# Optimization experiments

Hardware: AMD Instinct MI355X
Metric: run time of the kernel (lower is better)

Reference implementation:

```python
import jax, jax.numpy as jnp
import numpy as np

B, T, C = 2, 8192, 1024
H, BS, LW = 16, 64, 128          # num_heads, block_size, local_window_size
D = C // H                        # head_dim = 64
W = BS + LW                       # max window length per block = 192
NB = T // BS                      # number of blocks


def setup_inputs() -> dict:
    key = jax.random.key(0)
    ks = jax.random.split(key, 11)
    s = 1.0 / np.sqrt(C)          # small init so softmax is not saturated
    return {
        'query': jax.random.normal(ks[0], (B, T, C), jnp.float32),
        'key':   jax.random.normal(ks[1], (B, T, C), jnp.float32),
        'value': jax.random.normal(ks[2], (B, T, C), jnp.float32),
        'Wq': jax.random.normal(ks[3], (C, C), jnp.float32) * s,
        'bq': jax.random.normal(ks[4], (C,), jnp.float32) * s,
        'Wk': jax.random.normal(ks[5], (C, C), jnp.float32) * s,
        'bk': jax.random.normal(ks[6], (C,), jnp.float32) * s,
        'Wv': jax.random.normal(ks[7], (C, C), jnp.float32) * s,
        'bv': jax.random.normal(ks[8], (C,), jnp.float32) * s,
        'Wo': jax.random.normal(ks[9], (C, C), jnp.float32) * s,
        'bo': jax.random.normal(ks[10], (C,), jnp.float32) * s,
    }


def reference(query, key, value, Wq, bq, Wk, bk, Wv, bv, Wo, bo):
    # projections -> (B, H, T, D)
    def proj(x, Wt, bt):
        return (x @ Wt.T + bt).reshape(B, T, H, D).transpose(0, 2, 1, 3)

    scale = jnp.asarray(D, query.dtype) ** -0.5
    q = proj(query, Wq, bq) * scale
    k = proj(key, Wk, bk)
    v = proj(value, Wv, bv)

    # per-block window indices: block i attends to [i - LW//2, i + BS + LW//2)
    starts = jnp.arange(NB) * BS                              # (NB,)
    idx = starts[:, None] + jnp.arange(-LW // 2, BS + LW // 2)  # (NB, W)
    valid = (idx >= 0) & (idx < T)                            # (NB, W)
    cidx = jnp.clip(idx, 0, T - 1)

    q_blk = q.reshape(B, H, NB, BS, D)
    k_win = k[:, :, cidx, :]                                  # (B, H, NB, W, D)
    v_win = v[:, :, cidx, :]

    scores = jnp.einsum('bhnqd,bhnkd->bhnqk', q_blk, k_win).astype(jnp.float32)
    scores = jnp.where(valid[None, None, :, None, :], scores, -jnp.inf)
    probs = jax.nn.softmax(scores, axis=-1).astype(q.dtype)

    out = jnp.einsum('bhnqk,bhnkd->bhnqd', probs, v_win)      # (B, H, NB, BS, D)
    out = out.reshape(B, H, T, D).transpose(0, 2, 1, 3).reshape(B, T, C)
    return out @ Wo.T + bo
```

## Files before the change

kernel.cpp:

```cpp
#include <hip/hip_runtime.h>
#include <hip/hip_bf16.h>
#include <type_traits>

#define BATCH 2
#define SEQ   8192
#define CH    1024
#define NH    16
#define BLK   64
#define WIN   192
#define NBL   128
#define DH    64
#define MR    (BATCH*SEQ)

typedef __bf16 bf16x8 __attribute__((ext_vector_type(8)));
typedef float  f32x4  __attribute__((ext_vector_type(4)));

__device__ __forceinline__ f32x4 zero4() {
    f32x4 z; z[0]=0.f; z[1]=0.f; z[2]=0.f; z[3]=0.f; return z;
}

union Pack8 { __hip_bfloat16 h[8]; uint4 u; };
union Pack4 { __hip_bfloat16 h[4]; uint2 u; };

typedef const __attribute__((address_space(1))) unsigned int* gas_ptr;
typedef       __attribute__((address_space(3))) unsigned int* las_ptr;

__device__ __forceinline__ void gload_lds16(const __hip_bfloat16* g, __hip_bfloat16* l) {
    __builtin_amdgcn_global_load_lds((gas_ptr)(const void*)g, (las_ptr)(void*)l, 16, 0, 0);
}

__device__ __forceinline__ int xcd_swz(int bid, int nwg) {
    return (bid & 7) * (nwg >> 3) + (bid >> 3);
}

__global__ __launch_bounds__(256) void pack_all(
    const float* __restrict__ q,  const float* __restrict__ k,
    const float* __restrict__ v,
    const float* __restrict__ wq, const float* __restrict__ wk,
    const float* __restrict__ wv, const float* __restrict__ wo,
    __hip_bfloat16* __restrict__ xq, __hip_bfloat16* __restrict__ xk,
    __hip_bfloat16* __restrict__ xv,
    __hip_bfloat16* __restrict__ wqb, __hip_bfloat16* __restrict__ wkb,
    __hip_bfloat16* __restrict__ wvb, __hip_bfloat16* __restrict__ wob)
{
    const int NA8B = (MR * CH / 8) / 256;
    const int NW8B = (CH * CH / 8) / 256;
    int bid = blockIdx.x;
    const float* src;
    __hip_bfloat16* dst;
    int rel;
    if (bid < 3 * NA8B) {
        int t = bid / NA8B; rel = bid - t * NA8B;
        src = (t == 0) ? q : (t == 1) ? k : v;
        dst = (t == 0) ? xq : (t == 1) ? xk : xv;
    } else {
        int b2 = bid - 3 * NA8B;
        int t = b2 / NW8B; rel = b2 - t * NW8B;
        src = (t == 0) ? wq : (t == 1) ? wk : (t == 2) ? wv : wo;
        dst = (t == 0) ? wqb : (t == 1) ? wkb : (t == 2) ? wvb : wob;
    }
    const int base = rel * 512;
    const float4* s = reinterpret_cast<const float4*>(src);
    uint2* d = reinterpret_cast<uint2*>(dst);
    float4 a = s[base + threadIdx.x];
    float4 b = s[base + 256 + threadIdx.x];
    Pack4 pa, pb;
    pa.h[0] = __float2bfloat16(a.x); pa.h[1] = __float2bfloat16(a.y);
    pa.h[2] = __float2bfloat16(a.z); pa.h[3] = __float2bfloat16(a.w);
    pb.h[0] = __float2bfloat16(b.x); pb.h[1] = __float2bfloat16(b.y);
    pb.h[2] = __float2bfloat16(b.z); pb.h[3] = __float2bfloat16(b.w);
    d[base + threadIdx.x]       = pa.u;
    d[base + 256 + threadIdx.x] = pb.u;
}


__device__ __forceinline__ void stage_half(
    const __hip_bfloat16* __restrict__ g, int goff,
    __hip_bfloat16* sm, int loff, int tid)
{
    gload_lds16(g + goff,            sm + loff + tid * 8);
    gload_lds16(g + goff + 128 * CH, sm + loff + (tid + 512) * 8);
}

#define SB0 __builtin_amdgcn_sched_barrier(0)
#define LGKM0 do { asm volatile("s_waitcnt lgkmcnt(0)" ::: "memory"); \
                   __builtin_amdgcn_sched_barrier(0); } while (0)
#define VMCNT(n) do { asm volatile("s_waitcnt vmcnt(" #n ")" ::: "memory"); \
                      __builtin_amdgcn_sched_barrier(0); } while (0)

template<int MH, bool RB>
__device__ __forceinline__ void phase_reads(
    const __hip_bfloat16* Ak, const __hip_bfloat16* Bk,
    int aoff, int boff, bf16x8 (&af)[4], bf16x8 (&bfk)[4])
{
    if constexpr (RB) {
        #pragma unroll
        for (int j = 0; j < 4; ++j)
            bfk[j] = *reinterpret_cast<const bf16x8*>(Bk + boff + j * 512);
    }
    #pragma unroll
    for (int i = 0; i < 4; ++i)
        af[i] = *reinterpret_cast<const bf16x8*>(Ak + aoff + (MH * 4 + i) * 512);
}

template<int MH>
__device__ __forceinline__ void phase_mfma16(
    const bf16x8 (&af)[4], const bf16x8 (&bfk)[4], f32x4 (&acc)[8][4])
{
    __builtin_amdgcn_s_setprio(1);
    #pragma unroll
    for (int i = 0; i < 4; ++i)
        #pragma unroll
        for (int j = 0; j < 4; ++j)
            acc[MH * 4 + i][j] = __builtin_amdgcn_mfma_f32_16x16x32_bf16(
                af[i], bfk[j], acc[MH * 4 + i][j], 0, 0, 0);
    __builtin_amdgcn_s_setprio(0);
}

template<typename OT>
__device__ __forceinline__ void gemm_body256(
    const __hip_bfloat16* __restrict__ A, const __hip_bfloat16* __restrict__ Wb,
    const float* __restrict__ bias, OT* __restrict__ out, float alpha,
    int m0, int n0, __hip_bfloat16* sm)
{
    const int tid  = threadIdx.x;
    const int wid  = tid >> 6;
    const int lane = tid & 63;
    const int quad = lane >> 4;
    const int l16  = lane & 15;
    const int wr   = wid >> 2, wc = wid & 3;

    const int r0 = tid >> 2;
    const int s0 = (tid & 3) ^ ((tid >> 3) & 3);
    const int offA0 = (m0 + r0) * CH + s0 * 8;
    const int offB0 = (n0 + r0) * CH + s0 * 8;

    const int cq   = quad ^ ((l16 >> 1) & 3);
    const int aoff = ((wr * 128 + l16) * 4 + cq) * 8;
    const int boff = ((wc * 64  + l16) * 4 + cq) * 8;

    f32x4 acc[8][4];
    #pragma unroll
    for (int i = 0; i < 8; ++i)
        #pragma unroll
        for (int j = 0; j < 4; ++j) acc[i][j] = zero4();

    stage_half(A,  offA0,      sm, 0,             tid);
    stage_half(Wb, offB0,      sm, 32768,         tid);
    stage_half(A,  offA0 + 32, sm, 8192,          tid);
    stage_half(Wb, offB0 + 32, sm, 32768 + 8192,  tid);
    VMCNT(4);
    __builtin_amdgcn_s_barrier();
    SB0;

    bf16x8 af[4], bfk[4];

    #pragma unroll 1
    for (int t = 0; t < 15; ++t) {
        const int cur = t & 1, nb = cur ^ 1;
        const int kn  = (t + 1) * 64;
        const __hip_bfloat16* As_ = sm + cur * 16384;
        const __hip_bfloat16* Bs_ = sm + 32768 + cur * 16384;

        phase_reads<0, true>(As_, Bs_, aoff, boff, af, bfk);
        stage_half(A, offA0 + kn, sm, nb * 16384, tid);
        SB0;
        __builtin_amdgcn_s_barrier();
        LGKM0;
        phase_mfma16<0>(af, bfk, acc);
        __builtin_amdgcn_s_barrier();

        phase_reads<1, false>(As_, Bs_, aoff, boff, af, bfk);
        stage_half(Wb, offB0 + kn, sm, 32768 + nb * 16384, tid);
        SB0;
        __builtin_amdgcn_s_barrier();
        LGKM0;
        phase_mfma16<1>(af, bfk, acc);
        VMCNT(4);
        __builtin_amdgcn_s_barrier();

        phase_reads<0, true>(As_ + 8192, Bs_ + 8192, aoff, boff, af, bfk);
        stage_half(A, offA0 + kn + 32, sm, nb * 16384 + 8192, tid);
        SB0;
        __builtin_amdgcn_s_barrier();
        LGKM0;
        phase_mfma16<0>(af, bfk, acc);
        __builtin_amdgcn_s_barrier();

        phase_reads<1, false>(As_ + 8192, Bs_ + 8192, aoff, boff, af, bfk);
        stage_half(Wb, offB0 + kn + 32, sm, 32768 + nb * 16384 + 8192, tid);
        SB0;
        __builtin_amdgcn_s_barrier();
        LGKM0;
        phase_mfma16<1>(af, bfk, acc);
        VMCNT(4);
        __builtin_amdgcn_s_barrier();
    }

    {
        const __hip_bfloat16* As_ = sm + 16384;
        const __hip_bfloat16* Bs_ = sm + 32768 + 16384;

        phase_reads<0, true>(As_, Bs_, aoff, boff, af, bfk);
        SB0;
        __builtin_amdgcn_s_barrier();
        LGKM0;
        phase_mfma16<0>(af, bfk, acc);
        __builtin_amdgcn_s_barrier();

        phase_reads<1, false>(As_, Bs_, aoff, boff, af, bfk);
        SB0;
        __builtin_amdgcn_s_barrier();
        LGKM0;
        phase_mfma16<1>(af, bfk, acc);
        VMCNT(0);
        __builtin_amdgcn_s_barrier();

        phase_reads<0, true>(As_ + 8192, Bs_ + 8192, aoff, boff, af, bfk);
        SB0;
        __builtin_amdgcn_s_barrier();
        LGKM0;
        phase_mfma16<0>(af, bfk, acc);
        __builtin_amdgcn_s_barrier();

        phase_reads<1, false>(As_ + 8192, Bs_ + 8192, aoff, boff, af, bfk);
        SB0;
        __builtin_amdgcn_s_barrier();
        LGKM0;
        phase_mfma16<1>(af, bfk, acc);
    }

    #pragma unroll
    for (int j = 0; j < 4; ++j) {
        const int col = n0 + wc * 64 + j * 16 + l16;
        const float bv = bias[col];
        #pragma unroll
        for (int i = 0; i < 8; ++i) {
            #pragma unroll
            for (int r = 0; r < 4; ++r) {
                const int row = m0 + wr * 128 + i * 16 + quad * 4 + r;
                float v = alpha * (acc[i][j][r] + bv);
                if constexpr (std::is_same<OT, float>::value)
                    out[(size_t)row * CH + col] = v;
                else
                    out[(size_t)row * CH + col] = __float2bfloat16(v);
            }
        }
    }
}

__device__ __forceinline__ void gemm_tile256(int& m0, int& n0) {
    int bid = blockIdx.y * 4 + blockIdx.x;
    int swz = (bid & 7) * 32 + (bid >> 3);
    m0 = (swz >> 2) * 256;
    n0 = (swz & 3) * 256;
}

__global__ __launch_bounds__(512, 2) void gemm_qk256(
    const __hip_bfloat16* __restrict__ A0, const __hip_bfloat16* __restrict__ W0,
    const float* __restrict__ b0, __hip_bfloat16* __restrict__ o0, float alpha0,
    const __hip_bfloat16* __restrict__ A1, const __hip_bfloat16* __restrict__ W1,
    const float* __restrict__ b1, __hip_bfloat16* __restrict__ o1)
{
    __shared__ alignas(16) __hip_bfloat16 sm[65536];
    int m0, n0; gemm_tile256(m0, n0);
    if (blockIdx.z == 0)
        gemm_body256<__hip_bfloat16>(A0, W0, b0, o0, alpha0, m0, n0, sm);
    else
        gemm_body256<__hip_bfloat16>(A1, W1, b1, o1, 1.0f, m0, n0, sm);
}

template<typename OT>
__global__ __launch_bounds__(512, 2) void gemm_one256(
    const __hip_bfloat16* __restrict__ A, const __hip_bfloat16* __restrict__ Wb,
    const float* __restrict__ bias, OT* __restrict__ out)
{
    __shared__ alignas(16) __hip_bfloat16 sm[65536];
    int m0, n0; gemm_tile256(m0, n0);
    gemm_body256<OT>(A, Wb, bias, out, 1.0f, m0, n0, sm);
}

__global__ __launch_bounds__(256, 3) void attn_kernel(
    const __hip_bfloat16* __restrict__ qg,
    const __hip_bfloat16* __restrict__ kg,
    const __hip_bfloat16* __restrict__ vg,
    __hip_bfloat16* __restrict__ ctx)
{
    __shared__ alignas(16) char smem[53248];
    auto ks = reinterpret_cast<__hip_bfloat16(*)[72]>(smem);
    auto vt = reinterpret_cast<__hip_bfloat16(*)[200]>(smem + 27648);
    auto ps = reinterpret_cast<__hip_bfloat16(*)[200]>(smem);

    const int blk = xcd_swz(blockIdx.x, BATCH * NH * NBL);
    const int n = blk & (NBL - 1);
    const int h = (blk >> 7) & (NH - 1);
    const int b = blk >> 11;
    const int t0  = n * BLK;
    const int kst = t0 - 64;
    const int tid = threadIdx.x;
    const size_t baseBH = (size_t)b * SEQ * CH + (size_t)h * DH;

    const int wid = tid >> 6, lane = tid & 63, quad = lane >> 4, l16 = lane & 15;

    const __hip_bfloat16* qrow = qg + baseBH + (size_t)(t0 + wid * 16 + l16) * CH + quad * 8;
    bf16x8 aq0 = *reinterpret_cast<const bf16x8*>(qrow);
    bf16x8 aq1 = *reinterpret_cast<const bf16x8*>(qrow + 32);

    uint4 vreg[6];
    int vj[6], vseg[6];
    #pragma unroll
    for (int it = 0; it < 6; it++) {
        int c = tid + it * 256;
        vj[it] = c % WIN; vseg[it] = c / WIN;
        int tr = kst + vj[it]; tr = tr < 0 ? 0 : (tr >= SEQ ? SEQ - 1 : tr);
        vreg[it] = *reinterpret_cast<const uint4*>(vg + baseBH + (size_t)tr * CH + vseg[it] * 8);
    }

    #pragma unroll
    for (int it = 0; it < 6; it++) {
        int c = tid + it * 256;
        int row = c >> 3, seg = c & 7;
        int tr = kst + row; tr = tr < 0 ? 0 : (tr >= SEQ ? SEQ - 1 : tr);
        *reinterpret_cast<uint4*>(&ks[row][seg * 8]) =
            *reinterpret_cast<const uint4*>(kg + baseBH + (size_t)tr * CH + seg * 8);
    }
    __syncthreads();

    f32x4 sc[12];
    #pragma unroll
    for (int j = 0; j < 12; j++) sc[j] = zero4();
    #pragma unroll
    for (int j = 0; j < 12; j++) {
        bf16x8 bk0 = *reinterpret_cast<const bf16x8*>(&ks[j * 16 + l16][quad * 8]);
        sc[j] = __builtin_amdgcn_mfma_f32_16x16x32_bf16(aq0, bk0, sc[j], 0, 0, 0);
        bf16x8 bk1 = *reinterpret_cast<const bf16x8*>(&ks[j * 16 + l16][32 + quad * 8]);
        sc[j] = __builtin_amdgcn_mfma_f32_16x16x32_bf16(aq1, bk1, sc[j], 0, 0, 0);
    }
    __syncthreads();

    #pragma unroll
    for (int it = 0; it < 6; it++) {
        Pack8 p; p.u = vreg[it];
        #pragma unroll
        for (int e = 0; e < 8; e++) vt[vseg[it] * 8 + e][vj[it]] = p.h[e];
    }

    #pragma unroll
    for (int r = 0; r < 4; r++) {
        float s[12];
        float mx = -3.0e38f;
        #pragma unroll
        for (int j = 0; j < 12; j++) {
            int col = j * 16 + l16;
            int tr = kst + col;
            bool valid = (tr >= 0) && (tr < SEQ);
            s[j] = valid ? sc[j][r] : -3.0e38f;
            mx = fmaxf(mx, s[j]);
        }
        #pragma unroll
        for (int o = 1; o < 16; o <<= 1) mx = fmaxf(mx, __shfl_xor(mx, o, 64));
        float sum = 0.f;
        #pragma unroll
        for (int j = 0; j < 12; j++) {
            float e = __expf(s[j] - mx);
            s[j] = e;
            sum += e;
        }
        #pragma unroll
        for (int o = 1; o < 16; o <<= 1) sum += __shfl_xor(sum, o, 64);
        const float inv = 1.f / sum;
        const int row = wid * 16 + quad * 4 + r;
        #pragma unroll
        for (int j = 0; j < 12; j++)
            ps[row][j * 16 + l16] = __float2bfloat16(s[j] * inv);
    }
    __syncthreads();

    f32x4 oa[4];
    #pragma unroll
    for (int j = 0; j < 4; j++) oa[j] = zero4();
    #pragma unroll
    for (int kk = 0; kk < 6; kk++) {
        bf16x8 ap = *reinterpret_cast<const bf16x8*>(&ps[wid * 16 + l16][kk * 32 + quad * 8]);
        #pragma unroll
        for (int j = 0; j < 4; j++) {
            bf16x8 bv = *reinterpret_cast<const bf16x8*>(&vt[j * 16 + l16][kk * 32 + quad * 8]);
            oa[j] = __builtin_amdgcn_mfma_f32_16x16x32_bf16(ap, bv, oa[j], 0, 0, 0);
        }
    }
    #pragma unroll
    for (int j = 0; j < 4; j++) {
        const int d = j * 16 + l16;
        #pragma unroll
        for (int r = 0; r < 4; r++) {
            const int i = wid * 16 + quad * 4 + r;
            ctx[baseBH + (size_t)(t0 + i) * CH + d] = __float2bfloat16(oa[j][r]);
        }
    }
}

extern "C" void kernel_launch(void* const* d_in, const int* in_sizes, int n_in,
                              void* d_out, int out_size, void* d_ws, size_t ws_size,
                              hipStream_t stream)
{
    const float* query = (const float*)d_in[0];
    const float* key_i = (const float*)d_in[1];
    const float* value = (const float*)d_in[2];
    const float* Wq = (const float*)d_in[3];
    const float* bq = (const float*)d_in[4];
    const float* Wk = (const float*)d_in[5];
    const float* bk = (const float*)d_in[6];
    const float* Wv = (const float*)d_in[7];
    const float* bv = (const float*)d_in[8];
    const float* Wo = (const float*)d_in[9];
    const float* bo = (const float*)d_in[10];
    float* out = (float*)d_out;

    const size_t NELEM = (size_t)MR * CH;
    const size_t WELEM = (size_t)CH * CH;

    __hip_bfloat16* S0 = (__hip_bfloat16*)d_ws;
    __hip_bfloat16* S1 = S0 + NELEM;
    __hip_bfloat16* S2 = S1 + NELEM;
    __hip_bfloat16* S3 = S2 + NELEM;
    __hip_bfloat16* wqb = S3;
    __hip_bfloat16* wkb = S3 + WELEM;
    __hip_bfloat16* wvb = S3 + 2 * WELEM;
    __hip_bfloat16* wob = S3 + 3 * WELEM;

    __hip_bfloat16* xq = (__hip_bfloat16*)d_out;
    __hip_bfloat16* xk = xq + NELEM;
    __hip_bfloat16* vb = (__hip_bfloat16*)d_out;
    __hip_bfloat16* qb = S1;
    __hip_bfloat16* kb = S2;
    __hip_bfloat16* cb = S0;

    const int NA8B = (int)((NELEM / 8) / 256);
    const int NW8B = (int)((WELEM / 8) / 256);

    pack_all<<<3 * NA8B + 4 * NW8B, 256, 0, stream>>>(
        query, key_i, value, Wq, Wk, Wv, Wo,
        xq, xk, S0, wqb, wkb, wvb, wob);

    dim3 ggrid(CH / 256, MR / 256);
    dim3 qkgrid(CH / 256, MR / 256, 2);

    gemm_qk256<<<qkgrid, 512, 0, stream>>>(xq, wqb, bq, qb, 0.125f,
                                           xk, wkb, bk, kb);
    gemm_one256<__hip_bfloat16><<<ggrid, 512, 0, stream>>>(S0, wvb, bv, vb);

    attn_kernel<<<BATCH * NH * NBL, 256, 0, stream>>>(qb, kb, vb, cb);

    gemm_one256<float><<<ggrid, 512, 0, stream>>>(cb, wob, bo, out);
}
```

Before: 425.3 us.

## Fuse fp32-to-bf16 activation conversion into projection GEMM A-tile staging

Result: slower. 451.7 us (+6.2%).

```diff
diff --git a/kernel.cpp b/kernel.cpp
--- a/kernel.cpp
+++ b/kernel.cpp
@@ -20,7 +20,6 @@
 }
 
 union Pack8 { __hip_bfloat16 h[8]; uint4 u; };
-union Pack4 { __hip_bfloat16 h[4]; uint2 u; };
 
 typedef const __attribute__((address_space(1))) unsigned int* gas_ptr;
 typedef       __attribute__((address_space(3))) unsigned int* las_ptr;
@@ -33,38 +32,23 @@
     return (bid & 7) * (nwg >> 3) + (bid >> 3);
 }
 
-__global__ __launch_bounds__(256) void pack_all(
-    const float* __restrict__ q,  const float* __restrict__ k,
-    const float* __restrict__ v,
+__global__ __launch_bounds__(256) void pack_w(
     const float* __restrict__ wq, const float* __restrict__ wk,
     const float* __restrict__ wv, const float* __restrict__ wo,
-    __hip_bfloat16* __restrict__ xq, __hip_bfloat16* __restrict__ xk,
-    __hip_bfloat16* __restrict__ xv,
     __hip_bfloat16* __restrict__ wqb, __hip_bfloat16* __restrict__ wkb,
     __hip_bfloat16* __restrict__ wvb, __hip_bfloat16* __restrict__ wob)
 {
-    const int NA8B = (MR * CH / 8) / 256;
     const int NW8B = (CH * CH / 8) / 256;
     int bid = blockIdx.x;
-    const float* src;
-    __hip_bfloat16* dst;
-    int rel;
-    if (bid < 3 * NA8B) {
-        int t = bid / NA8B; rel = bid - t * NA8B;
-        src = (t == 0) ? q : (t == 1) ? k : v;
-        dst = (t == 0) ? xq : (t == 1) ? xk : xv;
-    } else {
-        int b2 = bid - 3 * NA8B;
-        int t = b2 / NW8B; rel = b2 - t * NW8B;
-        src = (t == 0) ? wq : (t == 1) ? wk : (t == 2) ? wv : wo;
-        dst = (t == 0) ? wqb : (t == 1) ? wkb : (t == 2) ? wvb : wob;
-    }
+    int t = bid >> 9, rel = bid & (NW8B - 1);
+    const float* src = (t == 0) ? wq : (t == 1) ? wk : (t == 2) ? wv : wo;
+    __hip_bfloat16* dst = (t == 0) ? wqb : (t == 1) ? wkb : (t == 2) ? wvb : wob;
     const int base = rel * 512;
     const float4* s = reinterpret_cast<const float4*>(src);
     uint2* d = reinterpret_cast<uint2*>(dst);
     float4 a = s[base + threadIdx.x];
     float4 b = s[base + 256 + threadIdx.x];
-    Pack4 pa, pb;
+    union { __hip_bfloat16 h[4]; uint2 u; } pa, pb;
     pa.h[0] = __float2bfloat16(a.x); pa.h[1] = __float2bfloat16(a.y);
     pa.h[2] = __float2bfloat16(a.z); pa.h[3] = __float2bfloat16(a.w);
     pb.h[0] = __float2bfloat16(b.x); pb.h[1] = __float2bfloat16(b.y);
@@ -82,6 +66,31 @@
     gload_lds16(g + goff + 128 * CH, sm + loff + (tid + 512) * 8);
 }
 
+__device__ __forceinline__ void stageA32_load(
+    const float* __restrict__ g, int goff, float4 (&fr)[4])
+{
+    const float4* p0 = reinterpret_cast<const float4*>(g + goff);
+    const float4* p1 = reinterpret_cast<const float4*>(g + goff + 128 * CH);
+    fr[0] = p0[0]; fr[1] = p0[1];
+    fr[2] = p1[0]; fr[3] = p1[1];
+}
+
+__device__ __forceinline__ void stageA32_write(
+    const float4 (&fr)[4], __hip_bfloat16* sm, int loff, int tid)
+{
+    Pack8 pa, pb;
+    pa.h[0] = __float2bfloat16(fr[0].x); pa.h[1] = __float2bfloat16(fr[0].y);
+    pa.h[2] = __float2bfloat16(fr[0].z); pa.h[3] = __float2bfloat16(fr[0].w);
+    pa.h[4] = __float2bfloat16(fr[1].x); pa.h[5] = __float2bfloat16(fr[1].y);
+    pa.h[6] = __float2bfloat16(fr[1].z); pa.h[7] = __float2bfloat16(fr[1].w);
+    pb.h[0] = __float2bfloat16(fr[2].x); pb.h[1] = __float2bfloat16(fr[2].y);
+    pb.h[2] = __float2bfloat16(fr[2].z); pb.h[3] = __float2bfloat16(fr[2].w);
+    pb.h[4] = __float2bfloat16(fr[3].x); pb.h[5] = __float2bfloat16(fr[3].y);
+    pb.h[6] = __float2bfloat16(fr[3].z); pb.h[7] = __float2bfloat16(fr[3].w);
+    *reinterpret_cast<uint4*>(sm + loff + tid * 8)         = pa.u;
+    *reinterpret_cast<uint4*>(sm + loff + (tid + 512) * 8) = pb.u;
+}
+
 #define SB0 __builtin_amdgcn_sched_barrier(0)
 #define LGKM0 do { asm volatile("s_waitcnt lgkmcnt(0)" ::: "memory"); \
                    __builtin_amdgcn_sched_barrier(0); } while (0)
@@ -117,12 +126,14 @@
     __builtin_amdgcn_s_setprio(0);
 }
 
-template<typename OT>
+template<typename OT, typename AT>
 __device__ __forceinline__ void gemm_body256(
-    const __hip_bfloat16* __restrict__ A, const __hip_bfloat16* __restrict__ Wb,
+    const AT* __restrict__ A, const __hip_bfloat16* __restrict__ Wb,
     const float* __restrict__ bias, OT* __restrict__ out, float alpha,
     int m0, int n0, __hip_bfloat16* sm)
 {
+    constexpr bool A32 = std::is_same<AT, float>::value;
+
     const int tid  = threadIdx.x;
     const int wid  = tid >> 6;
     const int lane = tid & 63;
@@ -145,11 +156,24 @@
         #pragma unroll
         for (int j = 0; j < 4; ++j) acc[i][j] = zero4();
 
-    stage_half(A,  offA0,      sm, 0,             tid);
-    stage_half(Wb, offB0,      sm, 32768,         tid);
-    stage_half(A,  offA0 + 32, sm, 8192,          tid);
-    stage_half(Wb, offB0 + 32, sm, 32768 + 8192,  tid);
-    VMCNT(4);
+    float4 frA[4], frB[4];
+
+    if constexpr (A32) {
+        stageA32_load(A, offA0,      frA);
+        stageA32_load(A, offA0 + 32, frB);
+        stage_half(Wb, offB0,      sm, 32768,        tid);
+        stage_half(Wb, offB0 + 32, sm, 32768 + 8192, tid);
+        VMCNT(8);  stageA32_write(frA, sm, 0,    tid);
+        VMCNT(4);  stageA32_write(frB, sm, 8192, tid);
+        VMCNT(2);
+        LGKM0;
+    } else {
+        stage_half(A,  offA0,      sm, 0,             tid);
+        stage_half(Wb, offB0,      sm, 32768,         tid);
+        stage_half(A,  offA0 + 32, sm, 8192,          tid);
+        stage_half(Wb, offB0 + 32, sm, 32768 + 8192,  tid);
+        VMCNT(4);
+    }
     __builtin_amdgcn_s_barrier();
     SB0;
 
@@ -163,37 +187,57 @@
         const __hip_bfloat16* Bs_ = sm + 32768 + cur * 16384;
 
         phase_reads<0, true>(As_, Bs_, aoff, boff, af, bfk);
-        stage_half(A, offA0 + kn, sm, nb * 16384, tid);
+        if constexpr (A32) {
+            stageA32_load(A, offA0 + kn, frA);
+            stage_half(Wb, offB0 + kn, sm, 32768 + nb * 16384, tid);
+        } else {
+            stage_half(A, offA0 + kn, sm, nb * 16384, tid);
+        }
         SB0;
         __builtin_amdgcn_s_barrier();
         LGKM0;
         phase_mfma16<0>(af, bfk, acc);
         __builtin_amdgcn_s_barrier();
 
+        if constexpr (A32) {
+            VMCNT(2);
+            stageA32_write(frA, sm, nb * 16384, tid);
+        }
         phase_reads<1, false>(As_, Bs_, aoff, boff, af, bfk);
-        stage_half(Wb, offB0 + kn, sm, 32768 + nb * 16384, tid);
+        if constexpr (!A32)
+            stage_half(Wb, offB0 + kn, sm, 32768 + nb * 16384, tid);
         SB0;
         __builtin_amdgcn_s_barrier();
         LGKM0;
         phase_mfma16<1>(af, bfk, acc);
-        VMCNT(4);
+        if constexpr (!A32) VMCNT(4);
         __builtin_amdgcn_s_barrier();
 
         phase_reads<0, true>(As_ + 8192, Bs_ + 8192, aoff, boff, af, bfk);
-        stage_half(A, offA0 + kn + 32, sm, nb * 16384 + 8192, tid);
+        if constexpr (A32) {
+            stageA32_load(A, offA0 + kn + 32, frA);
+            stage_half(Wb, offB0 + kn + 32, sm, 32768 + nb * 16384 + 8192, tid);
+        } else {
+            stage_half(A, offA0 + kn + 32, sm, nb * 16384 + 8192, tid);
+        }
         SB0;
         __builtin_amdgcn_s_barrier();
         LGKM0;
         phase_mfma16<0>(af, bfk, acc);
         __builtin_amdgcn_s_barrier();
 
+        if constexpr (A32) {
+            VMCNT(2);
+            stageA32_write(frA, sm, nb * 16384 + 8192, tid);
+        }
         phase_reads<1, false>(As_ + 8192, Bs_ + 8192, aoff, boff, af, bfk);
-        stage_half(Wb, offB0 + kn + 32, sm, 32768 + nb * 16384 + 8192, tid);
+        if constexpr (!A32)
+            stage_half(Wb, offB0 + kn + 32, sm, 32768 + nb * 16384 + 8192, tid);
         SB0;
         __builtin_amdgcn_s_barrier();
         LGKM0;
         phase_mfma16<1>(af, bfk, acc);
-        VMCNT(4);
+        if constexpr (!A32) VMCNT(4);
         __builtin_amdgcn_s_barrier();
     }
 
@@ -208,12 +252,13 @@
         phase_mfma16<0>(af, bfk, acc);
         __builtin_amdgcn_s_barrier();
 
+        if constexpr (A32) VMCNT(0);
         phase_reads<1, false>(As_, Bs_, aoff, boff, af, bfk);
         SB0;
         __builtin_amdgcn_s_barrier();
         LGKM0;
         phase_mfma16<1>(af, bfk, acc);
-        VMCNT(0);
+        if constexpr (!A32) VMCNT(0);
         __builtin_amdgcn_s_barrier();
 
         phase_reads<0, true>(As_ + 8192, Bs_ + 8192, aoff, boff, af, bfk);
@@ -257,27 +302,35 @@
 }
 
 __global__ __launch_bounds__(512, 2) void gemm_qk256(
-    const __hip_bfloat16* __restrict__ A0, const __hip_bfloat16* __restrict__ W0,
+    const float* __restrict__ A0, const __hip_bfloat16* __restrict__ W0,
     const float* __restrict__ b0, __hip_bfloat16* __restrict__ o0, float alpha0,
-    const __hip_bfloat16* __restrict__ A1, const __hip_bfloat16* __restrict__ W1,
+    const float* __restrict__ A1, const __hip_bfloat16* __restrict__ W1,
     const float* __restrict__ b1, __hip_bfloat16* __restrict__ o1)
 {
     __shared__ alignas(16) __hip_bfloat16 sm[65536];
     int m0, n0; gemm_tile256(m0, n0);
     if (blockIdx.z == 0)
-        gemm_body256<__hip_bfloat16>(A0, W0, b0, o0, alpha0, m0, n0, sm);
+        gemm_body256<__hip_bfloat16, float>(A0, W0, b0, o0, alpha0, m0, n0, sm);
     else
-        gemm_body256<__hip_bfloat16>(A1, W1, b1, o1, 1.0f, m0, n0, sm);
-}
-
-template<typename OT>
-__global__ __launch_bounds__(512, 2) void gemm_one256(
-    const __hip_bfloat16* __restrict__ A, const __hip_bfloat16* __restrict__ Wb,
-    const float* __restrict__ bias, OT* __restrict__ out)
+        gemm_body256<__hip_bfloat16, float>(A1, W1, b1, o1, 1.0f, m0, n0, sm);
+}
+
+__global__ __launch_bounds__(512, 2) void gemm_v256(
+    const float* __restrict__ A, const __hip_bfloat16* __restrict__ Wb,
+    const float* __restrict__ bias, __hip_bfloat16* __restrict__ out)
 {
     __shared__ alignas(16) __hip_bfloat16 sm[65536];
     int m0, n0; gemm_tile256(m0, n0);
-    gemm_body256<OT>(A, Wb, bias, out, 1.0f, m0, n0, sm);
+    gemm_body256<__hip_bfloat16, float>(A, Wb, bias, out, 1.0f, m0, n0, sm);
+}
+
+__global__ __launch_bounds__(512, 2) void gemm_o256(
+    const __hip_bfloat16* __restrict__ A, const __hip_bfloat16* __restrict__ Wb,
+    const float* __restrict__ bias, float* __restrict__ out)
+{
+    __shared__ alignas(16) __hip_bfloat16 sm[65536];
+    int m0, n0; gemm_tile256(m0, n0);
+    gemm_body256<float, __hip_bfloat16>(A, Wb, bias, out, 1.0f, m0, n0, sm);
 }
 
 __global__ __launch_bounds__(256, 3) void attn_kernel(
@@ -428,28 +481,23 @@
     __hip_bfloat16* wvb = S3 + 2 * WELEM;
     __hip_bfloat16* wob = S3 + 3 * WELEM;
 
-    __hip_bfloat16* xq = (__hip_bfloat16*)d_out;
-    __hip_bfloat16* xk = xq + NELEM;
     __hip_bfloat16* vb = (__hip_bfloat16*)d_out;
     __hip_bfloat16* qb = S1;
     __hip_bfloat16* kb = S2;
     __hip_bfloat16* cb = S0;
 
-    const int NA8B = (int)((NELEM / 8) / 256);
     const int NW8B = (int)((WELEM / 8) / 256);
 
-    pack_all<<<3 * NA8B + 4 * NW8B, 256, 0, stream>>>(
-        query, key_i, value, Wq, Wk, Wv, Wo,
-        xq, xk, S0, wqb, wkb, wvb, wob);
+    pack_w<<<4 * NW8B, 256, 0, stream>>>(Wq, Wk, Wv, Wo, wqb, wkb, wvb, wob);
 
     dim3 ggrid(CH / 256, MR / 256);
     dim3 qkgrid(CH / 256, MR / 256, 2);
 
-    gemm_qk256<<<qkgrid, 512, 0, stream>>>(xq, wqb, bq, qb, 0.125f,
-                                           xk, wkb, bk, kb);
-    gemm_one256<__hip_bfloat16><<<ggrid, 512, 0, stream>>>(S0, wvb, bv, vb);
+    gemm_qk256<<<qkgrid, 512, 0, stream>>>(query, wqb, bq, qb, 0.125f,
+                                           key_i, wkb, bk, kb);
+    gemm_v256<<<ggrid, 512, 0, stream>>>(value, wvb, bv, vb);
 
     attn_kernel<<<BATCH * NH * NBL, 256, 0, stream>>>(qb, kb, vb, cb);
 
-    gemm_one256<float><<<ggrid, 512, 0, stream>>>(cb, wob, bo, out);
-}
+    gemm_o256<<<ggrid, 512, 0, stream>>>(cb, wob, bo, out);
+}
```
